# Performance work log

Measured on AMD Instinct MI355X. Metric: run time of the kernel, lower is better.

Reference implementation:

```python
import jax, jax.numpy as jnp
import numpy as np

B, N, C = 4, 1024, 1024
H = 16
HD = C // H
HID = 4 * C
EPS = 1e-5


def layernorm(x, g, b):
    mu = jnp.mean(x, axis=-1, keepdims=True)
    var = jnp.mean(jnp.square(x - mu), axis=-1, keepdims=True)
    return (x - mu) * jax.lax.rsqrt(var + EPS) * g + b


def setup_inputs() -> dict:
    key = jax.random.key(0)
    ks = jax.random.split(key, 16)
    s = lambda d: 1.0 / np.sqrt(d)
    return {
        "x": jax.random.normal(ks[0], (B, N, C), dtype=jnp.float32),
        "ln1_g": jnp.ones((C,), jnp.float32),
        "ln1_b": jnp.zeros((C,), jnp.float32),
        "qkv_w": jax.random.normal(ks[1], (3 * C, C), jnp.float32) * s(C),
        "proj_w": jax.random.normal(ks[2], (C, C), jnp.float32) * s(C),
        "proj_b": jnp.zeros((C,), jnp.float32),
        "gamma1": jnp.full((C,), 1e-5, jnp.float32),
        "ln2_g": jnp.ones((C,), jnp.float32),
        "ln2_b": jnp.zeros((C,), jnp.float32),
        "fc1_w": jax.random.normal(ks[3], (HID, C), jnp.float32) * s(C),
        "fc1_b": jnp.zeros((HID,), jnp.float32),
        "fc2_w": jax.random.normal(ks[4], (C, HID), jnp.float32) * s(HID),
        "fc2_b": jnp.zeros((C,), jnp.float32),
        "gamma2": jnp.full((C,), 1e-5, jnp.float32),
    }


def reference(x, ln1_g, ln1_b, qkv_w, proj_w, proj_b, gamma1,
              ln2_g, ln2_b, fc1_w, fc1_b, fc2_w, fc2_b, gamma2):
    # --- attention residual branch ---
    n1 = layernorm(x, ln1_g, ln1_b)                     # [B,N,C]
    qkv = jnp.einsum('bnc,oc->bno', n1, qkv_w)          # [B,N,3C]
    qkv = qkv.reshape(B, N, 3, H, HD).transpose(2, 0, 3, 1, 4)  # [3,B,H,N,HD]
    scale = HD ** -0.5
    q, k, v = qkv[0] * scale, qkv[1], qkv[2]
    attn = jax.nn.softmax(jnp.einsum('bhnd,bhmd->bhnm', q, k), axis=-1)  # [B,H,N,N]
    ao = jnp.einsum('bhnm,bhmd->bhnd', attn, v)         # [B,H,N,HD]
    ao = ao.transpose(0, 2, 1, 3).reshape(B, N, C)
    ao = jnp.einsum('bnc,oc->bno', ao, proj_w) + proj_b
    x = x + ao * gamma1
    # --- mlp residual branch ---
    n2 = layernorm(x, ln2_g, ln2_b)
    h = jax.nn.gelu(jnp.einsum('bnc,hc->bnh', n2, fc1_w) + fc1_b, approximate=False)
    m = jnp.einsum('bnh,ch->bnc', h, fc2_w) + fc2_b
    x = x + m * gamma2
    return x, attn
```

## Files before the change

kernel.cpp:

```cpp
#include <hip/hip_runtime.h>
#include <math.h>

typedef __attribute__((ext_vector_type(8))) short bf16x8;
typedef __attribute__((ext_vector_type(4))) short bf16x4;
typedef __attribute__((ext_vector_type(4))) float f32x4;

__device__ __forceinline__ unsigned short f2bf(float f) {
  unsigned u = __builtin_bit_cast(unsigned, f);
  u += 0x7fffu + ((u >> 16) & 1u);
  return (unsigned short)(u >> 16);
}

#define MFMA16(a, b, c) __builtin_amdgcn_mfma_f32_16x16x32_bf16((a), (b), (c), 0, 0, 0)

__device__ __forceinline__ void gload_lds16(const void* g, void* l) {
  __builtin_amdgcn_global_load_lds(
      (const __attribute__((address_space(1))) unsigned*)g,
      (__attribute__((address_space(3))) unsigned*)l, 16, 0, 0);
}

__device__ __forceinline__ int xcd_swz(int bid, int nwg) {
  int q = nwg >> 3, r = nwg & 7;
  int xcd = bid & 7, off = bid >> 3;
  return (xcd < r ? xcd * (q + 1) : r * (q + 1) + (xcd - r) * q) + off;
}

__global__ __launch_bounds__(256) void k_cvt4(
    const float* __restrict__ wq, const float* __restrict__ wp,
    const float* __restrict__ w1, const float* __restrict__ w2,
    unsigned short* __restrict__ oq, unsigned short* __restrict__ op,
    unsigned short* __restrict__ o1, unsigned short* __restrict__ o2) {
  int bid = blockIdx.x;
  const float* src; unsigned short* dst; int base;
  if (bid < 3072)      { src = wq; dst = oq; base = bid; }
  else if (bid < 4096) { src = wp; dst = op; base = bid - 3072; }
  else if (bid < 8192) { src = w1; dst = o1; base = bid - 4096; }
  else                 { src = w2; dst = o2; base = bid - 8192; }
  int i = base * 256 + threadIdx.x;
  float4 v = ((const float4*)src)[i];
  bf16x4 o;
  o[0] = (short)f2bf(v.x); o[1] = (short)f2bf(v.y);
  o[2] = (short)f2bf(v.z); o[3] = (short)f2bf(v.w);
  *(bf16x4*)(dst + (size_t)i * 4) = o;
}

__global__ __launch_bounds__(256) void k_ln(const float* __restrict__ x,
                                            const float* __restrict__ g,
                                            const float* __restrict__ b,
                                            unsigned short* __restrict__ out) {
  __shared__ float red[8];
  const int tid = threadIdx.x;
  const size_t row = blockIdx.x;
  float4 v = ((const float4*)(x + row * 1024))[tid];
  float s = v.x + v.y + v.z + v.w;
#pragma unroll
  for (int off = 32; off; off >>= 1) s += __shfl_xor(s, off);
  if ((tid & 63) == 0) red[tid >> 6] = s;
  __syncthreads();
  float mu = (red[0] + red[1] + red[2] + red[3]) * (1.0f / 1024.0f);
  float dx = v.x - mu, dy = v.y - mu, dz = v.z - mu, dw = v.w - mu;
  float s2 = dx * dx + dy * dy + dz * dz + dw * dw;
#pragma unroll
  for (int off = 32; off; off >>= 1) s2 += __shfl_xor(s2, off);
  if ((tid & 63) == 0) red[4 + (tid >> 6)] = s2;
  __syncthreads();
  float var = (red[4] + red[5] + red[6] + red[7]) * (1.0f / 1024.0f);
  float rstd = rsqrtf(var + 1e-5f);
  float4 gv = ((const float4*)g)[tid];
  float4 bv = ((const float4*)b)[tid];
  bf16x4 o;
  o[0] = (short)f2bf(dx * rstd * gv.x + bv.x);
  o[1] = (short)f2bf(dy * rstd * gv.y + bv.y);
  o[2] = (short)f2bf(dz * rstd * gv.z + bv.z);
  o[3] = (short)f2bf(dw * rstd * gv.w + bv.w);
  *(bf16x4*)(out + row * 1024 + tid * 4) = o;
}

template <int EPI>
__global__ __launch_bounds__(512, 2) void k_gemm256(
    const unsigned short* __restrict__ A, const unsigned short* __restrict__ Bw,
    int Ndim, int K, int nby,
    const float* __restrict__ bias,
    unsigned short* __restrict__ outb) {
  __shared__ __align__(16) unsigned short lds[2][2][16384];

  const int tid = threadIdx.x;
  const int wid = tid >> 6, lane = tid & 63;
  const int wm = wid >> 2, wn = wid & 3;
  const int lr = lane & 15, lhi = lane >> 4;

  const int nwg = gridDim.x;
  const int swz = xcd_swz(blockIdx.x, nwg);
  const int bcol = swz / nby, brow = swz % nby;

  const size_t a_base = (size_t)brow * 256 * K;
  const size_t b_base = (size_t)bcol * 256 * K;
  const int NT = K >> 6;

  auto STAGE = [&](int dbuf, int kt, int which) {
    int ktc = (kt < NT) ? kt : 0;
    int isB = which & 1;
    int odd = which >> 1;
    const unsigned short* src = isB ? (Bw + b_base) : (A + a_base);
    int col = (ktc << 6) + (((lane & 7) ^ ((lane >> 3) & 7)) << 3);
#pragma unroll
    for (int c = 0; c < 2; ++c) {
      int idx = (wid << 1) | c;
      int chunk = isB ? ((idx & 3) + ((idx >> 2) << 3) + (odd << 2))
                      : ((idx & 7) + ((idx >> 3) << 4) + (odd << 3));
      int row = (chunk << 3) + (lane >> 3);
      gload_lds16(src + (size_t)row * K + col,
                  &lds[dbuf][isB][chunk * 512 + lane * 8]);
    }
  };

  STAGE(0, 0, 0); STAGE(0, 0, 1); STAGE(0, 0, 2); STAGE(0, 0, 3);

  f32x4 acc[8][4] = {};
  bf16x8 aF0[4][2], aF1[4][2], bF0[2][2], bF1[2][2];

  const int colx0 = (lhi << 4) ^ ((lr & 7) << 4);
  const int colx1 = (64 + (lhi << 4)) ^ ((lr & 7) << 4);

  for (int t = 0; t < NT; ++t) {
    const int buf = t & 1;
    const char* sAb = (const char*)&lds[buf][0][0];
    const char* sBb = (const char*)&lds[buf][1][0];
#pragma unroll
    for (int q = 0; q < 4; ++q) {
      asm volatile("s_waitcnt vmcnt(6)" ::: "memory");
      __builtin_amdgcn_s_barrier();
      if (q == 0) {
#pragma unroll
        for (int m = 0; m < 4; ++m) {
          int ro = (wm * 128 + m * 16 + lr) * 128;
          aF0[m][0] = *(const bf16x8*)(sAb + ro + colx0);
          aF0[m][1] = *(const bf16x8*)(sAb + ro + colx1);
        }
      } else if (q == 1) {
#pragma unroll
        for (int n = 0; n < 2; ++n) {
          int ro = (wn * 64 + n * 16 + lr) * 128;
          bF0[n][0] = *(const bf16x8*)(sBb + ro + colx0);
          bF0[n][1] = *(const bf16x8*)(sBb + ro + colx1);
        }
      } else if (q == 2) {
#pragma unroll
        for (int m = 0; m < 4; ++m) {
          int ro = (wm * 128 + 64 + m * 16 + lr) * 128;
          aF1[m][0] = *(const bf16x8*)(sAb + ro + colx0);
          aF1[m][1] = *(const bf16x8*)(sAb + ro + colx1);
        }
      } else {
#pragma unroll
        for (int n = 0; n < 2; ++n) {
          int ro = (wn * 64 + 32 + n * 16 + lr) * 128;
          bF1[n][0] = *(const bf16x8*)(sBb + ro + colx0);
          bF1[n][1] = *(const bf16x8*)(sBb + ro + colx1);
        }
      }
      STAGE(buf ^ 1, t + 1, q);
      asm volatile("s_waitcnt lgkmcnt(0)" ::: "memory");
      __builtin_amdgcn_sched_barrier(0);
      __builtin_amdgcn_s_setprio(1);
      if (q == 0) {
        if (t > 0) {
#pragma unroll
          for (int m = 0; m < 4; ++m)
#pragma unroll
            for (int n = 0; n < 2; ++n)
#pragma unroll
              for (int kk = 0; kk < 2; ++kk)
                acc[4 + m][2 + n] = MFMA16(aF1[m][kk], bF1[n][kk], acc[4 + m][2 + n]);
        }
      } else if (q == 1) {
#pragma unroll
        for (int m = 0; m < 4; ++m)
#pragma unroll
          for (int n = 0; n < 2; ++n)
#pragma unroll
            for (int kk = 0; kk < 2; ++kk)
              acc[m][n] = MFMA16(aF0[m][kk], bF0[n][kk], acc[m][n]);
      } else if (q == 2) {
#pragma unroll
        for (int m = 0; m < 4; ++m)
#pragma unroll
          for (int n = 0; n < 2; ++n)
#pragma unroll
            for (int kk = 0; kk < 2; ++kk)
              acc[4 + m][n] = MFMA16(aF1[m][kk], bF0[n][kk], acc[4 + m][n]);
      } else {
#pragma unroll
        for (int m = 0; m < 4; ++m)
#pragma unroll
          for (int n = 0; n < 2; ++n)
#pragma unroll
            for (int kk = 0; kk < 2; ++kk)
              acc[m][2 + n] = MFMA16(aF0[m][kk], bF1[n][kk], acc[m][2 + n]);
      }
      __builtin_amdgcn_s_setprio(0);
    }
  }
#pragma unroll
  for (int m = 0; m < 4; ++m)
#pragma unroll
    for (int n = 0; n < 2; ++n)
#pragma unroll
      for (int kk = 0; kk < 2; ++kk)
        acc[4 + m][2 + n] = MFMA16(aF1[m][kk], bF1[n][kk], acc[4 + m][2 + n]);

#pragma unroll
  for (int m = 0; m < 8; ++m)
#pragma unroll
    for (int n = 0; n < 4; ++n) {
      int col = bcol * 256 + wn * 64 + n * 16 + lr;
      float bi = (EPI == 1) ? bias[col] : 0.0f;
#pragma unroll
      for (int r = 0; r < 4; ++r) {
        int row = brow * 256 + wm * 128 + m * 16 + lhi * 4 + r;
        float v = acc[m][n][r];
        if (EPI == 1) {
          v += bi;
          v = 0.5f * v * (1.0f + erff(v * 0.70710678118654752f));
        }
        outb[(size_t)row * Ndim + col] = f2bf(v);
      }
    }
}

__global__ __launch_bounds__(256) void k_gemm_bt2(
    const unsigned short* __restrict__ A, const unsigned short* __restrict__ Bw,
    int Ndim, int K, int nby,
    const float* __restrict__ bias, const float* __restrict__ gamma,
    const float* __restrict__ resid, float* __restrict__ outf) {
  __shared__ __align__(16) unsigned short sA[128 * 64];
  __shared__ __align__(16) unsigned short sB[128 * 64];
  const int tid = threadIdx.x;
  const int wid = tid >> 6, lane = tid & 63;
  const int wr = wid >> 1, wc = wid & 1;
  const int lr = lane & 15, lhi = lane >> 4;
  const int swz = xcd_swz(blockIdx.x, gridDim.x);
  const int bcol = swz / nby, brow = swz % nby;

  const size_t a_base = (size_t)brow * 128 * K;
  const size_t b_base = (size_t)bcol * 128 * K;
  const int srow = tid >> 3;
  const int scol = (tid & 7) * 8;

  f32x4 acc[4][4] = {};

  for (int k0 = 0; k0 < K; k0 += 64) {
    __syncthreads();
#pragma unroll
    for (int r = 0; r < 4; ++r) {
      int row = r * 32 + srow;
      gload_lds16(&A[a_base + (size_t)row * K + k0 + scol], &sA[row * 64 + scol]);
      gload_lds16(&Bw[b_base + (size_t)row * K + k0 + scol], &sB[row * 64 + scol]);
    }
    __syncthreads();
#pragma unroll
    for (int kk = 0; kk < 2; ++kk) {
      bf16x8 af[4], bfr[4];
#pragma unroll
      for (int i = 0; i < 4; ++i) {
        int ar = wr * 64 + i * 16 + lr;
        af[i] = *(const bf16x8*)&sA[ar * 64 + kk * 32 + lhi * 8];
        int br = wc * 64 + i * 16 + lr;
        bfr[i] = *(const bf16x8*)&sB[br * 64 + kk * 32 + lhi * 8];
      }
#pragma unroll
      for (int i = 0; i < 4; ++i)
#pragma unroll
        for (int j = 0; j < 4; ++j)
          acc[i][j] = MFMA16(af[i], bfr[j], acc[i][j]);
    }
  }

#pragma unroll
  for (int i = 0; i < 4; ++i)
#pragma unroll
    for (int j = 0; j < 4; ++j)
#pragma unroll
      for (int r = 0; r < 4; ++r) {
        int row = brow * 128 + wr * 64 + i * 16 + lhi * 4 + r;
        int col = bcol * 128 + wc * 64 + j * 16 + lr;
        float v = resid[(size_t)row * Ndim + col] + (acc[i][j][r] + bias[col]) * gamma[col];
        outf[(size_t)row * Ndim + col] = v;
      }
}

__global__ __launch_bounds__(256) void k_attn(const unsigned short* __restrict__ qkv,
                                              float* __restrict__ attn_out,
                                              unsigned short* __restrict__ ao) {
  __shared__ __align__(16) char smem[49152];
  __shared__ float red[2][4][32];

  const int tid = threadIdx.x;
  const int wid = tid >> 6, lane = tid & 63;
  const int lr = lane & 15, lhi = lane >> 4;
  const int q0 = blockIdx.x * 32;
  const int bh = blockIdx.y;
  const int b = bh >> 4, h = bh & 15;
  const size_t row0 = (size_t)b * 1024 * 3072;
  const int hcol = h * 64;

  bf16x8 af[2][2];
#pragma unroll
  for (int i = 0; i < 2; ++i)
#pragma unroll
    for (int kk = 0; kk < 2; ++kk)
      af[i][kk] = *(const bf16x8*)&qkv[row0 + (size_t)(q0 + i * 16 + lr) * 3072 +
                                       hcol + kk * 32 + lhi * 8];

  f32x4 acc[2][16] = {};
#pragma unroll
  for (int kk = 0; kk < 2; ++kk) {
#pragma unroll
    for (int j = 0; j < 16; ++j) {
      int m = wid * 256 + j * 16 + lr;
      bf16x8 bv = *(const bf16x8*)&qkv[row0 + (size_t)m * 3072 + 1024 +
                                       hcol + kk * 32 + lhi * 8];
      acc[0][j] = MFMA16(af[0][kk], bv, acc[0][j]);
      acc[1][j] = MFMA16(af[1][kk], bv, acc[1][j]);
    }
  }

  float mx[2][4], sm[2][4];
#pragma unroll
  for (int i = 0; i < 2; ++i)
#pragma unroll
    for (int r = 0; r < 4; ++r) {
      float m_ = -1e30f;
#pragma unroll
      for (int j = 0; j < 16; ++j) {
        acc[i][j][r] *= 0.125f;
        m_ = fmaxf(m_, acc[i][j][r]);
      }
#pragma unroll
      for (int off = 1; off < 16; off <<= 1) m_ = fmaxf(m_, __shfl_xor(m_, off));
      mx[i][r] = m_;
    }
  if (lr == 0) {
#pragma unroll
    for (int i = 0; i < 2; ++i)
#pragma unroll
      for (int r = 0; r < 4; ++r) red[0][wid][i * 16 + lhi * 4 + r] = mx[i][r];
  }
  __syncthreads();
#pragma unroll
  for (int i = 0; i < 2; ++i)
#pragma unroll
    for (int r = 0; r < 4; ++r) {
      int rl = i * 16 + lhi * 4 + r;
      float m_ = fmaxf(fmaxf(red[0][0][rl], red[0][1][rl]),
                       fmaxf(red[0][2][rl], red[0][3][rl]));
      float s_ = 0.f;
#pragma unroll
      for (int j = 0; j < 16; ++j) {
        float e = __expf(acc[i][j][r] - m_);
        acc[i][j][r] = e;
        s_ += e;
      }
#pragma unroll
      for (int off = 1; off < 16; off <<= 1) s_ += __shfl_xor(s_, off);
      sm[i][r] = s_;
    }
  if (lr == 0) {
#pragma unroll
    for (int i = 0; i < 2; ++i)
#pragma unroll
      for (int r = 0; r < 4; ++r) red[1][wid][i * 16 + lhi * 4 + r] = sm[i][r];
  }
  __syncthreads();

  float inv[2][4];
#pragma unroll
  for (int i = 0; i < 2; ++i)
#pragma unroll
    for (int r = 0; r < 4; ++r) {
      int rl = i * 16 + lhi * 4 + r;
      inv[i][r] = 1.0f / (red[1][0][rl] + red[1][1][rl] + red[1][2][rl] + red[1][3][rl]);
    }

  unsigned pb[2][16][2];
  {
    const size_t attn_base =
        (size_t)bh * 1024 * 1024 + ((size_t)q0) * 1024 + (size_t)(wid * 256);
#pragma unroll
    for (int i = 0; i < 2; ++i)
#pragma unroll
      for (int j = 0; j < 16; ++j) {
        float p0 = acc[i][j][0] * inv[i][0];
        float p1 = acc[i][j][1] * inv[i][1];
        float p2 = acc[i][j][2] * inv[i][2];
        float p3 = acc[i][j][3] * inv[i][3];
        size_t base = attn_base + (size_t)(i * 16 + lhi * 4) * 1024 + j * 16 + lr;
        attn_out[base] = p0;
        attn_out[base + 1024] = p1;
        attn_out[base + 2048] = p2;
        attn_out[base + 3072] = p3;
        pb[i][j][0] = (unsigned)f2bf(p0) | ((unsigned)f2bf(p1) << 16);
        pb[i][j][1] = (unsigned)f2bf(p2) | ((unsigned)f2bf(p3) << 16);
      }
  }

  char* sP = smem + wid * 4096;
  char* sV = smem + 16384 + wid * 8192;
  f32x4 oaccT[4][2] = {};

#pragma unroll
  for (int t = 0; t < 4; ++t) {
#pragma unroll
    for (int i = 0; i < 2; ++i)
#pragma unroll
      for (int jl = 0; jl < 4; ++jl) {
        int j = t * 4 + jl;
        int kvl2 = (jl * 16 + lr) * 2;
#pragma unroll
        for (int hp = 0; hp < 2; ++hp) {
          unsigned d = pb[i][j][hp];
          int qa = i * 16 + lhi * 4 + hp * 2;
          int qb = qa + 1;
          *(unsigned short*)(sP + qa * 128 + (kvl2 ^ ((qa & 7) << 4))) =
              (unsigned short)(d & 0xffff);
          *(unsigned short*)(sP + qb * 128 + (kvl2 ^ ((qb & 7) << 4))) =
              (unsigned short)(d >> 16);
        }
      }
    {
      int kvq = lane >> 2;
      int dq = (lane & 3) * 8;
#pragma unroll
      for (int rt = 0; rt < 2; ++rt)
#pragma unroll
        for (int dh = 0; dh < 2; ++dh) {
          int kvp2 = rt * 16 + kvq;
          int kvg = wid * 256 + t * 64 + kvp2 * 2;
          int d0 = dh * 32 + dq;
          bf16x8 v0 = *(const bf16x8*)&qkv[row0 + (size_t)kvg * 3072 + 2048 + hcol + d0];
          bf16x8 v1 = *(const bf16x8*)&qkv[row0 + (size_t)(kvg + 1) * 3072 + 2048 + hcol + d0];
#pragma unroll
          for (int e = 0; e < 8; ++e) {
            int d = d0 + e;
            unsigned dw = (unsigned)(unsigned short)v0[e] |
                          ((unsigned)(unsigned short)v1[e] << 16);
            *(unsigned*)(sV + d * 128 + ((kvp2 * 4) ^ ((d & 7) << 4))) = dw;
          }
        }
    }
#pragma unroll
    for (int c = 0; c < 2; ++c) {
      bf16x8 pf[2];
#pragma unroll
      for (int qt = 0; qt < 2; ++qt) {
        int q_ = qt * 16 + lr;
        pf[qt] = *(const bf16x8*)(sP + q_ * 128 + ((c * 64 + lhi * 16) ^ ((q_ & 7) << 4)));
      }
#pragma unroll
      for (int dt = 0; dt < 4; ++dt) {
        int d_ = dt * 16 + lr;
        bf16x8 vf = *(const bf16x8*)(sV + d_ * 128 + ((c * 64 + lhi * 16) ^ ((d_ & 7) << 4)));
        oaccT[dt][0] = MFMA16(vf, pf[0], oaccT[dt][0]);
        oaccT[dt][1] = MFMA16(vf, pf[1], oaccT[dt][1]);
      }
    }
  }

  __syncthreads();
  float* sAO = (float*)smem;
#pragma unroll
  for (int dt = 0; dt < 4; ++dt)
#pragma unroll
    for (int qt = 0; qt < 2; ++qt)
#pragma unroll
      for (int r = 0; r < 4; ++r) {
        int q_ = qt * 16 + lr;
        int d_ = dt * 16 + lhi * 4 + r;
        sAO[wid * 2080 + q_ * 65 + d_] = oaccT[dt][qt][r];
      }
  __syncthreads();
  {
    int q_ = tid >> 3;
    int d0 = (tid & 7) * 8;
    bf16x8 o;
#pragma unroll
    for (int e = 0; e < 8; ++e) {
      int d_ = d0 + e;
      float s = sAO[q_ * 65 + d_] + sAO[2080 + q_ * 65 + d_] +
                sAO[4160 + q_ * 65 + d_] + sAO[6240 + q_ * 65 + d_];
      o[e] = (short)f2bf(s);
    }
    *(bf16x8*)&ao[(size_t)(b * 1024 + q0 + q_) * 1024 + hcol + d0] = o;
  }
}

extern "C" void kernel_launch(void* const* d_in, const int* in_sizes, int n_in,
                              void* d_out, int out_size, void* d_ws, size_t ws_size,
                              hipStream_t stream) {
  (void)in_sizes; (void)n_in; (void)out_size; (void)ws_size;
  const float* x     = (const float*)d_in[0];
  const float* ln1g  = (const float*)d_in[1];
  const float* ln1b  = (const float*)d_in[2];
  const float* qkvw  = (const float*)d_in[3];
  const float* projw = (const float*)d_in[4];
  const float* projb = (const float*)d_in[5];
  const float* g1    = (const float*)d_in[6];
  const float* ln2g  = (const float*)d_in[7];
  const float* ln2b  = (const float*)d_in[8];
  const float* fc1w  = (const float*)d_in[9];
  const float* fc1b  = (const float*)d_in[10];
  const float* fc2w  = (const float*)d_in[11];
  const float* fc2b  = (const float*)d_in[12];
  const float* g2    = (const float*)d_in[13];

  char* ws = (char*)d_ws;
  unsigned short* w_qkv  = (unsigned short*)(ws);
  unsigned short* w_proj = (unsigned short*)(ws + 6291456);
  unsigned short* w_fc1  = (unsigned short*)(ws + 8388608);
  unsigned short* w_fc2  = (unsigned short*)(ws + 16777216);
  unsigned short* n12    = (unsigned short*)(ws + 25165824);
  unsigned short* qkvb   = (unsigned short*)(ws + 33554432);
  unsigned short* hbuf   = qkvb;
  unsigned short* aob    = (unsigned short*)(ws + 58720256);
  float*          x1     = (float*)(ws + 67108864);

  float* outx = (float*)d_out;
  float* outattn = outx + (size_t)4096 * 1024;

  k_cvt4<<<12288, 256, 0, stream>>>(qkvw, projw, fc1w, fc2w,
                                    w_qkv, w_proj, w_fc1, w_fc2);

  k_ln<<<4096, 256, 0, stream>>>(x, ln1g, ln1b, n12);
  k_gemm256<0><<<192, 512, 0, stream>>>(n12, w_qkv, 3072, 1024, 16,
                                        nullptr, qkvb);
  k_attn<<<dim3(32, 64), 256, 0, stream>>>(qkvb, outattn, aob);
  k_gemm_bt2<<<256, 256, 0, stream>>>(aob, w_proj, 1024, 1024, 32,
                                      projb, g1, x, x1);
  k_ln<<<4096, 256, 0, stream>>>(x1, ln2g, ln2b, n12);
  k_gemm256<1><<<256, 512, 0, stream>>>(n12, w_fc1, 4096, 1024, 16,
                                        fc1b, hbuf);
  k_gemm_bt2<<<256, 256, 0, stream>>>(hbuf, w_fc2, 1024, 4096, 32,
                                      fc2b, g2, x1, outx);
}
```

Measured before the change: 377.4 us.

## Write QKV GEMM output head-major with transposed V for attention

The QKV GEMM epilogue now scatters Q and K into contiguous per-(batch,head) [N,64] buffers and writes V transposed as [64,N] per head. The attention kernel then reads K and V fragments straight from global memory and no longer stages V through LDS with a per-element transpose, which frees LDS and removes that shuffle work. In exchange the GEMM epilogue does less coalesced scattered stores, especially the 4-element V transposed writes, and V is now read directly from global or L2 rather than LDS.

```diff
diff --git a/kernel.cpp b/kernel.cpp
--- a/kernel.cpp
+++ b/kernel.cpp
@@ -81,6 +81,8 @@
     const unsigned short* __restrict__ A, const unsigned short* __restrict__ Bw,
     int Ndim, int K, int nby,
     const float* __restrict__ bias,
+    unsigned short* __restrict__ Qc, unsigned short* __restrict__ Kc,
+    unsigned short* __restrict__ VTo,
     unsigned short* __restrict__ outb) {
   __shared__ __align__(16) unsigned short lds[2][2][16384];
 
@@ -209,23 +211,56 @@
       for (int kk = 0; kk < 2; ++kk)
         acc[4 + m][2 + n] = MFMA16(aF1[m][kk], bF1[n][kk], acc[4 + m][2 + n]);
 
-#pragma unroll
-  for (int m = 0; m < 8; ++m)
-#pragma unroll
-    for (int n = 0; n < 4; ++n) {
-      int col = bcol * 256 + wn * 64 + n * 16 + lr;
-      float bi = (EPI == 1) ? bias[col] : 0.0f;
-#pragma unroll
-      for (int r = 0; r < 4; ++r) {
-        int row = brow * 256 + wm * 128 + m * 16 + lhi * 4 + r;
-        float v = acc[m][n][r];
-        if (EPI == 1) {
-          v += bi;
+  if (EPI == 0) {
+    const int region = bcol >> 2;
+    const int h = (bcol & 3) * 4 + wn;
+    if (region < 2) {
+      unsigned short* dst = (region == 0) ? Qc : Kc;
+#pragma unroll
+      for (int m = 0; m < 8; ++m)
+#pragma unroll
+        for (int n = 0; n < 4; ++n) {
+          int d = n * 16 + lr;
+#pragma unroll
+          for (int r = 0; r < 4; ++r) {
+            int row = brow * 256 + wm * 128 + m * 16 + lhi * 4 + r;
+            int b = row >> 10, kv = row & 1023;
+            dst[((size_t)((b << 4) + h) << 16) + (size_t)kv * 64 + d] =
+                f2bf(acc[m][n][r]);
+          }
+        }
+    } else {
+#pragma unroll
+      for (int m = 0; m < 8; ++m)
+#pragma unroll
+        for (int n = 0; n < 4; ++n) {
+          int d = n * 16 + lr;
+          int row0_ = brow * 256 + wm * 128 + m * 16 + lhi * 4;
+          int b = row0_ >> 10, kv0 = row0_ & 1023;
+          bf16x4 o;
+          o[0] = (short)f2bf(acc[m][n][0]);
+          o[1] = (short)f2bf(acc[m][n][1]);
+          o[2] = (short)f2bf(acc[m][n][2]);
+          o[3] = (short)f2bf(acc[m][n][3]);
+          *(bf16x4*)&VTo[((size_t)((b << 4) + h) << 16) + ((size_t)d << 10) + kv0] = o;
+        }
+    }
+  } else {
+#pragma unroll
+    for (int m = 0; m < 8; ++m)
+#pragma unroll
+      for (int n = 0; n < 4; ++n) {
+        int col = bcol * 256 + wn * 64 + n * 16 + lr;
+        float bi = bias[col];
+#pragma unroll
+        for (int r = 0; r < 4; ++r) {
+          int row = brow * 256 + wm * 128 + m * 16 + lhi * 4 + r;
+          float v = acc[m][n][r] + bi;
           v = 0.5f * v * (1.0f + erff(v * 0.70710678118654752f));
-        }
-        outb[(size_t)row * Ndim + col] = f2bf(v);
-      }
-    }
+          outb[(size_t)row * Ndim + col] = f2bf(v);
+        }
+      }
+  }
 }
 
 __global__ __launch_bounds__(256) void k_gemm_bt2(
@@ -289,10 +324,12 @@
       }
 }
 
-__global__ __launch_bounds__(256) void k_attn(const unsigned short* __restrict__ qkv,
+__global__ __launch_bounds__(256) void k_attn(const unsigned short* __restrict__ Qc,
+                                              const unsigned short* __restrict__ Kc,
+                                              const unsigned short* __restrict__ VT,
                                               float* __restrict__ attn_out,
                                               unsigned short* __restrict__ ao) {
-  __shared__ __align__(16) char smem[49152];
+  __shared__ __align__(16) char smem[33280];
   __shared__ float red[2][4][32];
 
   const int tid = threadIdx.x;
@@ -301,7 +338,7 @@
   const int q0 = blockIdx.x * 32;
   const int bh = blockIdx.y;
   const int b = bh >> 4, h = bh & 15;
-  const size_t row0 = (size_t)b * 1024 * 3072;
+  const size_t hb = (size_t)bh << 16;
   const int hcol = h * 64;
 
   bf16x8 af[2][2];
@@ -309,8 +346,8 @@
   for (int i = 0; i < 2; ++i)
 #pragma unroll
     for (int kk = 0; kk < 2; ++kk)
-      af[i][kk] = *(const bf16x8*)&qkv[row0 + (size_t)(q0 + i * 16 + lr) * 3072 +
-                                       hcol + kk * 32 + lhi * 8];
+      af[i][kk] = *(const bf16x8*)&Qc[hb + (size_t)(q0 + i * 16 + lr) * 64 +
+                                      kk * 32 + lhi * 8];
 
   f32x4 acc[2][16] = {};
 #pragma unroll
@@ -318,8 +355,7 @@
 #pragma unroll
     for (int j = 0; j < 16; ++j) {
       int m = wid * 256 + j * 16 + lr;
-      bf16x8 bv = *(const bf16x8*)&qkv[row0 + (size_t)m * 3072 + 1024 +
-                                       hcol + kk * 32 + lhi * 8];
+      bf16x8 bv = *(const bf16x8*)&Kc[hb + (size_t)m * 64 + kk * 32 + lhi * 8];
       acc[0][j] = MFMA16(af[0][kk], bv, acc[0][j]);
       acc[1][j] = MFMA16(af[1][kk], bv, acc[1][j]);
     }
@@ -405,7 +441,6 @@
   }
 
   char* sP = smem + wid * 4096;
-  char* sV = smem + 16384 + wid * 8192;
   f32x4 oaccT[4][2] = {};
 
 #pragma unroll
@@ -427,27 +462,6 @@
               (unsigned short)(d >> 16);
         }
       }
-    {
-      int kvq = lane >> 2;
-      int dq = (lane & 3) * 8;
-#pragma unroll
-      for (int rt = 0; rt < 2; ++rt)
-#pragma unroll
-        for (int dh = 0; dh < 2; ++dh) {
-          int kvp2 = rt * 16 + kvq;
-          int kvg = wid * 256 + t * 64 + kvp2 * 2;
-          int d0 = dh * 32 + dq;
-          bf16x8 v0 = *(const bf16x8*)&qkv[row0 + (size_t)kvg * 3072 + 2048 + hcol + d0];
-          bf16x8 v1 = *(const bf16x8*)&qkv[row0 + (size_t)(kvg + 1) * 3072 + 2048 + hcol + d0];
-#pragma unroll
-          for (int e = 0; e < 8; ++e) {
-            int d = d0 + e;
-            unsigned dw = (unsigned)(unsigned short)v0[e] |
-                          ((unsigned)(unsigned short)v1[e] << 16);
-            *(unsigned*)(sV + d * 128 + ((kvp2 * 4) ^ ((d & 7) << 4))) = dw;
-          }
-        }
-    }
 #pragma unroll
     for (int c = 0; c < 2; ++c) {
       bf16x8 pf[2];
@@ -459,7 +473,8 @@
 #pragma unroll
       for (int dt = 0; dt < 4; ++dt) {
         int d_ = dt * 16 + lr;
-        bf16x8 vf = *(const bf16x8*)(sV + d_ * 128 + ((c * 64 + lhi * 16) ^ ((d_ & 7) << 4)));
+        bf16x8 vf = *(const bf16x8*)&VT[hb + ((size_t)d_ << 10) +
+                                        wid * 256 + t * 64 + c * 32 + lhi * 8];
         oaccT[dt][0] = MFMA16(vf, pf[0], oaccT[dt][0]);
         oaccT[dt][1] = MFMA16(vf, pf[1], oaccT[dt][1]);
       }
@@ -519,8 +534,10 @@
   unsigned short* w_fc1  = (unsigned short*)(ws + 8388608);
   unsigned short* w_fc2  = (unsigned short*)(ws + 16777216);
   unsigned short* n12    = (unsigned short*)(ws + 25165824);
-  unsigned short* qkvb   = (unsigned short*)(ws + 33554432);
-  unsigned short* hbuf   = qkvb;
+  unsigned short* Qc     = (unsigned short*)(ws + 33554432);
+  unsigned short* Kc     = (unsigned short*)(ws + 41943040);
+  unsigned short* VT     = (unsigned short*)(ws + 50331648);
+  unsigned short* hbuf   = (unsigned short*)(ws + 33554432);
   unsigned short* aob    = (unsigned short*)(ws + 58720256);
   float*          x1     = (float*)(ws + 67108864);
 
@@ -532,13 +549,13 @@
 
   k_ln<<<4096, 256, 0, stream>>>(x, ln1g, ln1b, n12);
   k_gemm256<0><<<192, 512, 0, stream>>>(n12, w_qkv, 3072, 1024, 16,
-                                        nullptr, qkvb);
-  k_attn<<<dim3(32, 64), 256, 0, stream>>>(qkvb, outattn, aob);
+                                        nullptr, Qc, Kc, VT, nullptr);
+  k_attn<<<dim3(32, 64), 256, 0, stream>>>(Qc, Kc, VT, outattn, aob);
   k_gemm_bt2<<<256, 256, 0, stream>>>(aob, w_proj, 1024, 1024, 32,
                                       projb, g1, x, x1);
   k_ln<<<4096, 256, 0, stream>>>(x1, ln2g, ln2b, n12);
   k_gemm256<1><<<256, 512, 0, stream>>>(n12, w_fc1, 4096, 1024, 16,
-                                        fc1b, hbuf);
+                                        fc1b, nullptr, nullptr, nullptr, hbuf);
   k_gemm_bt2<<<256, 256, 0, stream>>>(hbuf, w_fc2, 1024, 4096, 32,
                                       fc2b, g2, x1, outx);
 }
```

Measured after the change: 379.7 us. About the same (+0.6%).
